# Performance work log

Measured on AMD Instinct MI355X. Metric: run time of the kernel, lower is better.

Reference implementation:

```python
import jax, jax.numpy as jnp
import numpy as np

CUTOFF = 5.2
BOX = 44.0
N_ATOMS = 8192

# 13 half-shifts used by the cell list (vector_index_displacement) + zero shift
HALF_SHIFTS = np.array([
    [-1, 0, 0], [-1, -1, 0], [0, -1, 0], [1, -1, 0],
    [-1, 1, -1], [0, 1, -1], [1, 1, -1], [-1, 0, -1],
    [0, 0, -1], [1, 0, -1], [-1, -1, -1], [0, -1, -1], [1, -1, -1]], dtype=np.int64)
ALL_SHIFTS = np.concatenate([np.zeros((1, 3), dtype=np.int64), HALF_SHIFTS], axis=0)  # (14,3)


def setup_inputs() -> dict:
    key = jax.random.key(0)
    k1, k2 = jax.random.split(key)
    species = jax.random.randint(k1, (1, N_ATOMS), 0, 4, dtype=jnp.int64)
    coordinates = jax.random.uniform(k2, (1, N_ATOMS, 3), dtype=jnp.float32) * BOX
    cell = jnp.eye(3, dtype=jnp.float32) * BOX
    pbc = jnp.ones((3,), dtype=bool)
    return {"species": species, "coordinates": coordinates, "cell": cell, "pbc": pbc}


def reference(species, coordinates, cell, pbc):
    # Single molecule, as asserted by the torch module.
    coords = coordinates[0]  # (N, 3)
    n = coords.shape[0]
    # map_to_central: wrap coordinates into the central cell
    frac = coords @ jnp.linalg.inv(cell)
    frac = frac - jnp.floor(frac)
    coords = frac @ cell
    # orthorhombic cell diagonal (norm of cell columns, as in _setup_variables)
    diag = jnp.linalg.norm(cell, axis=0)  # (3,)

    shifts = jnp.asarray(ALL_SHIFTS)
    pairs_list, shift_list = [], []
    cutoff2 = CUTOFF * CUTOFF
    for k in range(shifts.shape[0]):  # fixed small loop over 14 periodic shifts
        s = shifts[k]
        # delta[i, j] = r_i - r_j + s * cell_diagonal   (N, N, 3)
        delta = coords[:, None, :] - coords[None, :, :] + s.astype(coords.dtype) * diag
        d2 = jnp.sum(delta * delta, axis=-1)  # (N, N)
        mask = d2 <= cutoff2
        if k == 0:
            # within-image pairs: each unordered pair once, no self pairs
            mask = jnp.triu(mask, 1)
        i, j = jnp.nonzero(mask)  # eager: data-dependent pair count
        pairs_list.append(jnp.stack([i, j], axis=0))
        shift_list.append(jnp.broadcast_to(s, (i.shape[0], 3)))
    atom_pairs = jnp.concatenate(pairs_list, axis=1)  # (2, P)
    shift_indices = jnp.concatenate(shift_list, axis=0)  # (P, 3)
    return atom_pairs, shift_indices


if __name__ == "__main__":
    out = reference(**setup_inputs())
    print(out[0].shape, out[1].shape)
```

## Files before the change

### kernel.cpp

```cpp
#include <hip/hip_runtime.h>

#define CLD_NATOMS 8192
#define CLD_NSHIFT 14
#define CLD_NROWS (CLD_NSHIFT * CLD_NATOMS)
#define CLD_NTILE 112
#define CLD_NCELL 512
#define CLD_CAP 128
#define CLD_C2 ((float)(5.2 * 5.2))
#define CLD_R 5.35f

__device__ const int cld_shifts[CLD_NSHIFT][3] = {
    {0, 0, 0},
    {-1, 0, 0}, {-1, -1, 0}, {0, -1, 0}, {1, -1, 0},
    {-1, 1, -1}, {0, 1, -1}, {1, 1, -1}, {-1, 0, -1},
    {0, 0, -1}, {1, 0, -1}, {-1, -1, -1}, {0, -1, -1}, {1, -1, -1}};

__device__ float4 cld_pp[CLD_NATOMS];
__device__ int cld_cid[CLD_NATOMS];
__device__ float4 cld_sorted[CLD_NATOMS];
__device__ unsigned cld_cstart[CLD_NCELL + 1];
__device__ unsigned cld_cfill[CLD_NCELL];
__device__ int cld_jbuf[(size_t)CLD_NROWS * CLD_CAP];
__device__ unsigned cld_cnt[CLD_NROWS];
__device__ unsigned cld_off[CLD_NROWS];
__device__ unsigned cld_tot[CLD_NTILE];
__device__ float4 cld_dg;
__device__ float4 cld_cinv;
__device__ float4 cld_sf[CLD_NSHIFT];

__global__ __launch_bounds__(256) void cld_wrapbin(const float* __restrict__ coords,
                                                   const float* __restrict__ cell) {
  int i = blockIdx.x * blockDim.x + threadIdx.x;
  if (i >= CLD_NATOMS) return;
  float dgx = (float)sqrt((double)cell[0] * cell[0] + (double)cell[3] * cell[3] +
                          (double)cell[6] * cell[6]);
  float dgy = (float)sqrt((double)cell[1] * cell[1] + (double)cell[4] * cell[4] +
                          (double)cell[7] * cell[7]);
  float dgz = (float)sqrt((double)cell[2] * cell[2] + (double)cell[5] * cell[5] +
                          (double)cell[8] * cell[8]);
  float cix = 8.0f / dgx, ciy = 8.0f / dgy, ciz = 8.0f / dgz;
  if (i == 0) {
    cld_dg = make_float4(dgx, dgy, dgz, 0.f);
    cld_cinv = make_float4(cix, ciy, ciz, 0.f);
    for (int k = 0; k < CLD_NSHIFT; ++k)
      cld_sf[k] = make_float4(__fmul_rn((float)cld_shifts[k][0], dgx),
                              __fmul_rn((float)cld_shifts[k][1], dgy),
                              __fmul_rn((float)cld_shifts[k][2], dgz), 0.f);
  }

  double a00 = cell[0], a01 = cell[1], a02 = cell[2];
  double a10 = cell[3], a11 = cell[4], a12 = cell[5];
  double a20 = cell[6], a21 = cell[7], a22 = cell[8];
  double det = a00 * (a11 * a22 - a12 * a21) - a01 * (a10 * a22 - a12 * a20) +
               a02 * (a10 * a21 - a11 * a20);
  double id = 1.0 / det;
  float inv[3][3];
  inv[0][0] = (float)((a11 * a22 - a12 * a21) * id);
  inv[0][1] = (float)(-(a01 * a22 - a02 * a21) * id);
  inv[0][2] = (float)((a01 * a12 - a02 * a11) * id);
  inv[1][0] = (float)(-(a10 * a22 - a12 * a20) * id);
  inv[1][1] = (float)((a00 * a22 - a02 * a20) * id);
  inv[1][2] = (float)(-(a00 * a12 - a02 * a10) * id);
  inv[2][0] = (float)((a10 * a21 - a11 * a20) * id);
  inv[2][1] = (float)(-(a00 * a21 - a01 * a20) * id);
  inv[2][2] = (float)((a00 * a11 - a01 * a10) * id);

  float x = coords[3 * i], y = coords[3 * i + 1], z = coords[3 * i + 2];
  float fr[3], w[3];
#pragma unroll
  for (int c = 0; c < 3; ++c) {
    float f = __fadd_rn(__fadd_rn(__fmul_rn(x, inv[0][c]), __fmul_rn(y, inv[1][c])),
                        __fmul_rn(z, inv[2][c]));
    fr[c] = __fsub_rn(f, floorf(f));
  }
#pragma unroll
  for (int c = 0; c < 3; ++c) {
    w[c] = __fadd_rn(
        __fadd_rn(__fmul_rn(fr[0], cell[0 * 3 + c]), __fmul_rn(fr[1], cell[1 * 3 + c])),
        __fmul_rn(fr[2], cell[2 * 3 + c]));
  }
  cld_pp[i] = make_float4(w[0], w[1], w[2], 0.0f);
  int cx = min(7, (int)(w[0] * cix));
  int cy = min(7, (int)(w[1] * ciy));
  int cz = min(7, (int)(w[2] * ciz));
  cld_cid[i] = (cz * 8 + cy) * 8 + cx;
}

__global__ __launch_bounds__(1024) void cld_cscan() {
  __shared__ unsigned h[CLD_NCELL];
  int t = threadIdx.x;
  if (t < CLD_NCELL) h[t] = 0u;
  __syncthreads();
#pragma unroll
  for (int r = 0; r < 8; ++r) atomicAdd(&h[cld_cid[t + r * 1024]], 1u);
  __syncthreads();
  unsigned v = (t < CLD_NCELL) ? h[t] : 0u;
  unsigned acc = v;
  for (int off = 1; off < CLD_NCELL; off <<= 1) {
    unsigned a = (t >= off && t < CLD_NCELL) ? h[t - off] : 0u;
    __syncthreads();
    if (t < CLD_NCELL) {
      acc += a;
      h[t] = acc;
    }
    __syncthreads();
  }
  if (t < CLD_NCELL) {
    cld_cstart[t] = acc - v;
    cld_cfill[t] = acc - v;
  }
  if (t == CLD_NCELL - 1) cld_cstart[CLD_NCELL] = acc;
}

__global__ __launch_bounds__(256) void cld_scatter() {
  int i = blockIdx.x * blockDim.x + threadIdx.x;
  if (i >= CLD_NATOMS) return;
  unsigned pos = atomicAdd(&cld_cfill[cld_cid[i]], 1u);
  float4 p = cld_pp[i];
  p.w = __int_as_float(i);
  cld_sorted[pos] = p;
}

__device__ __forceinline__ bool cld_alive(float xi, float yi, float zi, int sx, int sy,
                                          int sz, float dgx, float dgy, float dgz) {
  bool a = true;
  if (sx < 0) a = a && (xi >= dgx - 5.3f); else if (sx > 0) a = a && (xi <= 5.3f);
  if (sy < 0) a = a && (yi >= dgy - 5.3f); else if (sy > 0) a = a && (yi <= 5.3f);
  if (sz < 0) a = a && (zi >= dgz - 5.3f); else if (sz > 0) a = a && (zi <= 5.3f);
  return a;
}

__device__ __forceinline__ void cld_crange(float t, float ci, int& lo, int& hi) {
  lo = max(0, (int)(fmaxf(t - CLD_R, 0.f) * ci));
  hi = min(7, (int)(fmaxf(t + CLD_R, 0.f) * ci));
}

__device__ __forceinline__ unsigned cld_iscan(unsigned v, int lane) {
  for (int off = 1; off < 64; off <<= 1) {
    unsigned t = __shfl_up(v, off);
    if (lane >= off) v += t;
  }
  return v;
}

__global__ __launch_bounds__(512) void cld_count() {
  __shared__ uint4 smask[8][64];
  int wslot = threadIdx.x >> 6;
  int wv = blockIdx.x * 8 + wslot;
  int lane = threadIdx.x & 63;
  unsigned* lm = (unsigned*)smask[wslot];
  int k = wv >> 13, i = wv & (CLD_NATOMS - 1);

  float4 dg = cld_dg;
  float4 sc = cld_sf[k];
  int sx = cld_shifts[k][0], sy = cld_shifts[k][1], sz = cld_shifts[k][2];
  float4 pi = cld_pp[i];
  if (k != 0 && !cld_alive(pi.x, pi.y, pi.z, sx, sy, sz, dg.x, dg.y, dg.z)) {
    if (lane == 0) cld_cnt[wv] = 0u;
    return;
  }
  smask[wslot][lane] = make_uint4(0u, 0u, 0u, 0u);

  float4 cinv = cld_cinv;
  int xlo, xhi, ylo, yhi, zlo, zhi;
  cld_crange(__fadd_rn(pi.x, sc.x), cinv.x, xlo, xhi);
  cld_crange(__fadd_rn(pi.y, sc.y), cinv.y, ylo, yhi);
  cld_crange(__fadd_rn(pi.z, sc.z), cinv.z, zlo, zhi);

  for (int cz = zlo; cz <= zhi; ++cz) {
    for (int cy = ylo; cy <= yhi; ++cy) {
      int idb = (cz * 8 + cy) * 8;
      unsigned b = cld_cstart[idb + xlo], e = cld_cstart[idb + xhi + 1];
      for (unsigned t = b + lane; t < e; t += 64) {
        float4 pj = cld_sorted[t];
        int j = __float_as_int(pj.w);
        float dx = __fadd_rn(__fsub_rn(pi.x, pj.x), sc.x);
        float dy = __fadd_rn(__fsub_rn(pi.y, pj.y), sc.y);
        float dz = __fadd_rn(__fsub_rn(pi.z, pj.z), sc.z);
        float d2 = __fadd_rn(__fadd_rn(__fmul_rn(dx, dx), __fmul_rn(dy, dy)),
                             __fmul_rn(dz, dz));
        bool ok = (d2 <= CLD_C2) && (k != 0 || i < j);
        if (ok) atomicOr(&lm[(unsigned)j >> 5], 1u << (j & 31));
      }
    }
  }
  __threadfence_block();

  const unsigned long long* mrow = (const unsigned long long*)lm;
  unsigned long long m0 = mrow[lane];
  unsigned long long m1 = mrow[64 + lane];
  unsigned c0 = (unsigned)__popcll(m0), c1 = (unsigned)__popcll(m1);
  unsigned s0 = cld_iscan(c0, lane);
  unsigned T0 = __shfl(s0, 63);
  unsigned e0 = s0 - c0;
  unsigned s1 = cld_iscan(c1, lane);
  unsigned T1 = __shfl(s1, 63);
  unsigned e1 = T0 + s1 - c1;

  size_t jb = (size_t)wv * CLD_CAP;
  unsigned p = e0;
  unsigned long long m = m0;
  while (m) {
    int b = __ffsll((long long)m) - 1;
    m &= m - 1;
    if (p < CLD_CAP) cld_jbuf[jb + p] = (lane << 6) + b;
    ++p;
  }
  p = e1;
  m = m1;
  while (m) {
    int b = __ffsll((long long)m) - 1;
    m &= m - 1;
    if (p < CLD_CAP) cld_jbuf[jb + p] = ((64 + lane) << 6) + b;
    ++p;
  }
  if (lane == 0) cld_cnt[wv] = min(T0 + T1, (unsigned)CLD_CAP);
}

__global__ __launch_bounds__(1024) void cld_s1() {
  __shared__ unsigned sd[1024];
  int t = threadIdx.x;
  int gid = blockIdx.x * 1024 + t;
  unsigned v = cld_cnt[gid];
  sd[t] = v;
  __syncthreads();
  unsigned acc = v;
  for (int off = 1; off < 1024; off <<= 1) {
    unsigned a = (t >= off) ? sd[t - off] : 0u;
    __syncthreads();
    acc += a;
    sd[t] = acc;
    __syncthreads();
  }
  cld_off[gid] = acc - v;
  if (t == 1023) cld_tot[blockIdx.x] = acc;
}

__global__ __launch_bounds__(512) void cld_emit(int* __restrict__ out, int P) {
  int wv = blockIdx.x * 8 + (threadIdx.x >> 6);
  int lane = threadIdx.x & 63;
  unsigned c = cld_cnt[wv];
  if (c == 0) return;
  int tile = wv >> 10;
  unsigned v = 0;
  if (lane < tile) v = cld_tot[lane];
  if (64 + lane < tile) v += cld_tot[64 + lane];
#pragma unroll
  for (int off = 32; off; off >>= 1) v += __shfl_down(v, off);
  unsigned tbase = __shfl(v, 0);

  unsigned off0 = cld_off[wv] + tbase;
  int k = wv >> 13, i = wv & (CLD_NATOMS - 1);
  int sx = cld_shifts[k][0], sy = cld_shifts[k][1], sz = cld_shifts[k][2];
  size_t jb = (size_t)wv * CLD_CAP;
  for (unsigned q = lane; q < c; q += 64) {
    unsigned p = off0 + q;
    if (p < (unsigned)P) {
      out[p] = i;
      out[P + p] = cld_jbuf[jb + q];
      unsigned sp = 2u * (unsigned)P + 3u * p;
      out[sp] = sx;
      out[sp + 1] = sy;
      out[sp + 2] = sz;
    }
  }
}

extern "C" void kernel_launch(void* const* d_in, const int* in_sizes, int n_in,
                              void* d_out, int out_size, void* d_ws, size_t ws_size,
                              hipStream_t stream) {
  const float* coords = (const float*)d_in[1];
  const float* cell = (const float*)d_in[2];
  int P = out_size / 5;

  cld_wrapbin<<<CLD_NATOMS / 256, 256, 0, stream>>>(coords, cell);
  cld_cscan<<<1, 1024, 0, stream>>>();
  cld_scatter<<<CLD_NATOMS / 256, 256, 0, stream>>>();
  cld_count<<<CLD_NROWS / 8, 512, 0, stream>>>();
  cld_s1<<<CLD_NTILE, 1024, 0, stream>>>();
  cld_emit<<<CLD_NROWS / 8, 512, 0, stream>>>((int*)d_out, P);
}
```

Measured before the change: 53.24 us.

## Compact alive (shift, atom) rows into a work list and use persistent waves

The scatter kernel now evaluates the periodic-boundary liveness test for every shift and appends the surviving rows to a global list with an atomic counter. The count and emit kernels run a fixed grid of persistent waves that stride over this compacted list, so they no longer launch one wave per row across all 14 shifts. Counts are zeroed up front in the wrap kernel so dead rows still scan correctly. The intent is to cut launch and early-exit overhead for the many dead rows. The cost is an extra global atomic plus list writes, and row order in the list is nondeterministic, though output offsets still come from the row-indexed scan.

```diff
diff --git a/kernel.cpp b/kernel.cpp
--- a/kernel.cpp
+++ b/kernel.cpp
@@ -1,37 +1,49 @@
 #include <hip/hip_runtime.h>
 
-#define CLD_NATOMS 8192
-#define CLD_NSHIFT 14
-#define CLD_NROWS (CLD_NSHIFT * CLD_NATOMS)
-#define CLD_NTILE 112
-#define CLD_NCELL 512
-#define CLD_CAP 128
-#define CLD_C2 ((float)(5.2 * 5.2))
-#define CLD_R 5.35f
-
-__device__ const int cld_shifts[CLD_NSHIFT][3] = {
+#define CLF_NATOMS 8192
+#define CLF_NSHIFT 14
+#define CLF_NROWS (CLF_NSHIFT * CLF_NATOMS)
+#define CLF_NTILE 112
+#define CLF_NCELL 512
+#define CLF_CAP 128
+#define CLF_PWAVES 8192
+#define CLF_C2 ((float)(5.2 * 5.2))
+#define CLF_R 5.35f
+
+__device__ const int clf_shifts[CLF_NSHIFT][3] = {
     {0, 0, 0},
     {-1, 0, 0}, {-1, -1, 0}, {0, -1, 0}, {1, -1, 0},
     {-1, 1, -1}, {0, 1, -1}, {1, 1, -1}, {-1, 0, -1},
     {0, 0, -1}, {1, 0, -1}, {-1, -1, -1}, {0, -1, -1}, {1, -1, -1}};
 
-__device__ float4 cld_pp[CLD_NATOMS];
-__device__ int cld_cid[CLD_NATOMS];
-__device__ float4 cld_sorted[CLD_NATOMS];
-__device__ unsigned cld_cstart[CLD_NCELL + 1];
-__device__ unsigned cld_cfill[CLD_NCELL];
-__device__ int cld_jbuf[(size_t)CLD_NROWS * CLD_CAP];
-__device__ unsigned cld_cnt[CLD_NROWS];
-__device__ unsigned cld_off[CLD_NROWS];
-__device__ unsigned cld_tot[CLD_NTILE];
-__device__ float4 cld_dg;
-__device__ float4 cld_cinv;
-__device__ float4 cld_sf[CLD_NSHIFT];
-
-__global__ __launch_bounds__(256) void cld_wrapbin(const float* __restrict__ coords,
+__device__ float4 clf_pp[CLF_NATOMS];
+__device__ int clf_cid[CLF_NATOMS];
+__device__ float4 clf_sorted[CLF_NATOMS];
+__device__ unsigned clf_cstart[CLF_NCELL + 1];
+__device__ unsigned clf_cfill[CLF_NCELL];
+__device__ unsigned clf_nalive;
+__device__ unsigned clf_alist[CLF_NROWS];
+__device__ int clf_jbuf[(size_t)CLF_NROWS * CLF_CAP];
+__device__ unsigned clf_cnt[CLF_NROWS];
+__device__ unsigned clf_off[CLF_NROWS];
+__device__ unsigned clf_tot[CLF_NTILE];
+__device__ float4 clf_dg;
+__device__ float4 clf_cinv;
+__device__ float4 clf_sf[CLF_NSHIFT];
+
+__device__ __forceinline__ bool clf_alive(float xi, float yi, float zi, int sx, int sy,
+                                          int sz, float dgx, float dgy, float dgz) {
+  bool a = true;
+  if (sx < 0) a = a && (xi >= dgx - 5.3f); else if (sx > 0) a = a && (xi <= 5.3f);
+  if (sy < 0) a = a && (yi >= dgy - 5.3f); else if (sy > 0) a = a && (yi <= 5.3f);
+  if (sz < 0) a = a && (zi >= dgz - 5.3f); else if (sz > 0) a = a && (zi <= 5.3f);
+  return a;
+}
+
+__global__ __launch_bounds__(256) void clf_wrapbin(const float* __restrict__ coords,
                                                    const float* __restrict__ cell) {
   int i = blockIdx.x * blockDim.x + threadIdx.x;
-  if (i >= CLD_NATOMS) return;
+  if (i >= CLF_NATOMS) return;
   float dgx = (float)sqrt((double)cell[0] * cell[0] + (double)cell[3] * cell[3] +
                           (double)cell[6] * cell[6]);
   float dgy = (float)sqrt((double)cell[1] * cell[1] + (double)cell[4] * cell[4] +
@@ -40,13 +52,16 @@
                           (double)cell[8] * cell[8]);
   float cix = 8.0f / dgx, ciy = 8.0f / dgy, ciz = 8.0f / dgz;
   if (i == 0) {
-    cld_dg = make_float4(dgx, dgy, dgz, 0.f);
-    cld_cinv = make_float4(cix, ciy, ciz, 0.f);
-    for (int k = 0; k < CLD_NSHIFT; ++k)
-      cld_sf[k] = make_float4(__fmul_rn((float)cld_shifts[k][0], dgx),
-                              __fmul_rn((float)cld_shifts[k][1], dgy),
-                              __fmul_rn((float)cld_shifts[k][2], dgz), 0.f);
-  }
+    clf_dg = make_float4(dgx, dgy, dgz, 0.f);
+    clf_cinv = make_float4(cix, ciy, ciz, 0.f);
+    clf_nalive = 0u;
+    for (int k = 0; k < CLF_NSHIFT; ++k)
+      clf_sf[k] = make_float4(__fmul_rn((float)clf_shifts[k][0], dgx),
+                              __fmul_rn((float)clf_shifts[k][1], dgy),
+                              __fmul_rn((float)clf_shifts[k][2], dgz), 0.f);
+  }
+#pragma unroll
+  for (int k = 0; k < CLF_NSHIFT; ++k) clf_cnt[(k << 13) + i] = 0u;
 
   double a00 = cell[0], a01 = cell[1], a02 = cell[2];
   double a10 = cell[3], a11 = cell[4], a12 = cell[5];
@@ -79,63 +94,68 @@
         __fadd_rn(__fmul_rn(fr[0], cell[0 * 3 + c]), __fmul_rn(fr[1], cell[1 * 3 + c])),
         __fmul_rn(fr[2], cell[2 * 3 + c]));
   }
-  cld_pp[i] = make_float4(w[0], w[1], w[2], 0.0f);
+  clf_pp[i] = make_float4(w[0], w[1], w[2], 0.0f);
   int cx = min(7, (int)(w[0] * cix));
   int cy = min(7, (int)(w[1] * ciy));
   int cz = min(7, (int)(w[2] * ciz));
-  cld_cid[i] = (cz * 8 + cy) * 8 + cx;
-}
-
-__global__ __launch_bounds__(1024) void cld_cscan() {
-  __shared__ unsigned h[CLD_NCELL];
+  clf_cid[i] = (cz * 8 + cy) * 8 + cx;
+}
+
+__global__ __launch_bounds__(1024) void clf_cscan() {
+  __shared__ unsigned h[CLF_NCELL];
   int t = threadIdx.x;
-  if (t < CLD_NCELL) h[t] = 0u;
+  if (t < CLF_NCELL) h[t] = 0u;
   __syncthreads();
 #pragma unroll
-  for (int r = 0; r < 8; ++r) atomicAdd(&h[cld_cid[t + r * 1024]], 1u);
+  for (int r = 0; r < 8; ++r) atomicAdd(&h[clf_cid[t + r * 1024]], 1u);
   __syncthreads();
-  unsigned v = (t < CLD_NCELL) ? h[t] : 0u;
+  unsigned v = (t < CLF_NCELL) ? h[t] : 0u;
   unsigned acc = v;
-  for (int off = 1; off < CLD_NCELL; off <<= 1) {
-    unsigned a = (t >= off && t < CLD_NCELL) ? h[t - off] : 0u;
+  for (int off = 1; off < CLF_NCELL; off <<= 1) {
+    unsigned a = (t >= off && t < CLF_NCELL) ? h[t - off] : 0u;
     __syncthreads();
-    if (t < CLD_NCELL) {
+    if (t < CLF_NCELL) {
       acc += a;
       h[t] = acc;
     }
     __syncthreads();
   }
-  if (t < CLD_NCELL) {
-    cld_cstart[t] = acc - v;
-    cld_cfill[t] = acc - v;
-  }
-  if (t == CLD_NCELL - 1) cld_cstart[CLD_NCELL] = acc;
-}
-
-__global__ __launch_bounds__(256) void cld_scatter() {
+  if (t < CLF_NCELL) {
+    clf_cstart[t] = acc - v;
+    clf_cfill[t] = acc - v;
+  }
+  if (t == CLF_NCELL - 1) clf_cstart[CLF_NCELL] = acc;
+}
+
+__global__ __launch_bounds__(256) void clf_scatter() {
   int i = blockIdx.x * blockDim.x + threadIdx.x;
-  if (i >= CLD_NATOMS) return;
-  unsigned pos = atomicAdd(&cld_cfill[cld_cid[i]], 1u);
-  float4 p = cld_pp[i];
-  p.w = __int_as_float(i);
-  cld_sorted[pos] = p;
-}
-
-__device__ __forceinline__ bool cld_alive(float xi, float yi, float zi, int sx, int sy,
-                                          int sz, float dgx, float dgy, float dgz) {
-  bool a = true;
-  if (sx < 0) a = a && (xi >= dgx - 5.3f); else if (sx > 0) a = a && (xi <= 5.3f);
-  if (sy < 0) a = a && (yi >= dgy - 5.3f); else if (sy > 0) a = a && (yi <= 5.3f);
-  if (sz < 0) a = a && (zi >= dgz - 5.3f); else if (sz > 0) a = a && (zi <= 5.3f);
-  return a;
-}
-
-__device__ __forceinline__ void cld_crange(float t, float ci, int& lo, int& hi) {
-  lo = max(0, (int)(fmaxf(t - CLD_R, 0.f) * ci));
-  hi = min(7, (int)(fmaxf(t + CLD_R, 0.f) * ci));
-}
-
-__device__ __forceinline__ unsigned cld_iscan(unsigned v, int lane) {
+  if (i >= CLF_NATOMS) return;
+  float4 p = clf_pp[i];
+  unsigned pos = atomicAdd(&clf_cfill[clf_cid[i]], 1u);
+  float4 ps = p;
+  ps.w = __int_as_float(i);
+  clf_sorted[pos] = ps;
+
+  float4 dg = clf_dg;
+  unsigned rows[CLF_NSHIFT];
+  int m = 0;
+  rows[m++] = (unsigned)i;
+#pragma unroll
+  for (int k = 1; k < CLF_NSHIFT; ++k) {
+    if (clf_alive(p.x, p.y, p.z, clf_shifts[k][0], clf_shifts[k][1], clf_shifts[k][2],
+                  dg.x, dg.y, dg.z))
+      rows[m++] = (unsigned)((k << 13) + i);
+  }
+  unsigned base = atomicAdd(&clf_nalive, (unsigned)m);
+  for (int q = 0; q < m; ++q) clf_alist[base + q] = rows[q];
+}
+
+__device__ __forceinline__ void clf_crange(float t, float ci, int& lo, int& hi) {
+  lo = max(0, (int)(fmaxf(t - CLF_R, 0.f) * ci));
+  hi = min(7, (int)(fmaxf(t + CLF_R, 0.f) * ci));
+}
+
+__device__ __forceinline__ unsigned clf_iscan(unsigned v, int lane) {
   for (int off = 1; off < 64; off <<= 1) {
     unsigned t = __shfl_up(v, off);
     if (lane >= off) v += t;
@@ -143,85 +163,85 @@
   return v;
 }
 
-__global__ __launch_bounds__(512) void cld_count() {
+__global__ __launch_bounds__(512) void clf_count() {
   __shared__ uint4 smask[8][64];
   int wslot = threadIdx.x >> 6;
-  int wv = blockIdx.x * 8 + wslot;
   int lane = threadIdx.x & 63;
   unsigned* lm = (unsigned*)smask[wslot];
-  int k = wv >> 13, i = wv & (CLD_NATOMS - 1);
-
-  float4 dg = cld_dg;
-  float4 sc = cld_sf[k];
-  int sx = cld_shifts[k][0], sy = cld_shifts[k][1], sz = cld_shifts[k][2];
-  float4 pi = cld_pp[i];
-  if (k != 0 && !cld_alive(pi.x, pi.y, pi.z, sx, sy, sz, dg.x, dg.y, dg.z)) {
-    if (lane == 0) cld_cnt[wv] = 0u;
-    return;
-  }
-  smask[wslot][lane] = make_uint4(0u, 0u, 0u, 0u);
-
-  float4 cinv = cld_cinv;
-  int xlo, xhi, ylo, yhi, zlo, zhi;
-  cld_crange(__fadd_rn(pi.x, sc.x), cinv.x, xlo, xhi);
-  cld_crange(__fadd_rn(pi.y, sc.y), cinv.y, ylo, yhi);
-  cld_crange(__fadd_rn(pi.z, sc.z), cinv.z, zlo, zhi);
-
-  for (int cz = zlo; cz <= zhi; ++cz) {
-    for (int cy = ylo; cy <= yhi; ++cy) {
-      int idb = (cz * 8 + cy) * 8;
-      unsigned b = cld_cstart[idb + xlo], e = cld_cstart[idb + xhi + 1];
-      for (unsigned t = b + lane; t < e; t += 64) {
-        float4 pj = cld_sorted[t];
-        int j = __float_as_int(pj.w);
-        float dx = __fadd_rn(__fsub_rn(pi.x, pj.x), sc.x);
-        float dy = __fadd_rn(__fsub_rn(pi.y, pj.y), sc.y);
-        float dz = __fadd_rn(__fsub_rn(pi.z, pj.z), sc.z);
-        float d2 = __fadd_rn(__fadd_rn(__fmul_rn(dx, dx), __fmul_rn(dy, dy)),
-                             __fmul_rn(dz, dz));
-        bool ok = (d2 <= CLD_C2) && (k != 0 || i < j);
-        if (ok) atomicOr(&lm[(unsigned)j >> 5], 1u << (j & 31));
+  unsigned na = clf_nalive;
+
+  float4 cinv = clf_cinv;
+
+  for (unsigned w = blockIdx.x * 8 + wslot; w < na; w += CLF_PWAVES) {
+    unsigned row = clf_alist[w];
+    int k = row >> 13, i = row & (CLF_NATOMS - 1);
+    float4 sc = clf_sf[k];
+    float4 pi = clf_pp[i];
+    smask[wslot][lane] = make_uint4(0u, 0u, 0u, 0u);
+
+    int xlo, xhi, ylo, yhi, zlo, zhi;
+    clf_crange(__fadd_rn(pi.x, sc.x), cinv.x, xlo, xhi);
+    clf_crange(__fadd_rn(pi.y, sc.y), cinv.y, ylo, yhi);
+    clf_crange(__fadd_rn(pi.z, sc.z), cinv.z, zlo, zhi);
+
+    for (int cz = zlo; cz <= zhi; ++cz) {
+      for (int cy = ylo; cy <= yhi; ++cy) {
+        int idb = (cz * 8 + cy) * 8;
+        unsigned b = clf_cstart[idb + xlo], e = clf_cstart[idb + xhi + 1];
+        for (unsigned t = b + lane; t < e; t += 64) {
+          float4 pj = clf_sorted[t];
+          int j = __float_as_int(pj.w);
+          float dx = __fadd_rn(__fsub_rn(pi.x, pj.x), sc.x);
+          float dy = __fadd_rn(__fsub_rn(pi.y, pj.y), sc.y);
+          float dz = __fadd_rn(__fsub_rn(pi.z, pj.z), sc.z);
+          float d2 = __fadd_rn(__fadd_rn(__fmul_rn(dx, dx), __fmul_rn(dy, dy)),
+                               __fmul_rn(dz, dz));
+          bool ok = (d2 <= CLF_C2) && (k != 0 || i < j);
+          if (ok) atomicOr(&lm[(unsigned)j >> 5], 1u << (j & 31));
+        }
       }
     }
-  }
-  __threadfence_block();
-
-  const unsigned long long* mrow = (const unsigned long long*)lm;
-  unsigned long long m0 = mrow[lane];
-  unsigned long long m1 = mrow[64 + lane];
-  unsigned c0 = (unsigned)__popcll(m0), c1 = (unsigned)__popcll(m1);
-  unsigned s0 = cld_iscan(c0, lane);
-  unsigned T0 = __shfl(s0, 63);
-  unsigned e0 = s0 - c0;
-  unsigned s1 = cld_iscan(c1, lane);
-  unsigned T1 = __shfl(s1, 63);
-  unsigned e1 = T0 + s1 - c1;
-
-  size_t jb = (size_t)wv * CLD_CAP;
-  unsigned p = e0;
-  unsigned long long m = m0;
-  while (m) {
-    int b = __ffsll((long long)m) - 1;
-    m &= m - 1;
-    if (p < CLD_CAP) cld_jbuf[jb + p] = (lane << 6) + b;
-    ++p;
-  }
-  p = e1;
-  m = m1;
-  while (m) {
-    int b = __ffsll((long long)m) - 1;
-    m &= m - 1;
-    if (p < CLD_CAP) cld_jbuf[jb + p] = ((64 + lane) << 6) + b;
-    ++p;
-  }
-  if (lane == 0) cld_cnt[wv] = min(T0 + T1, (unsigned)CLD_CAP);
-}
-
-__global__ __launch_bounds__(1024) void cld_s1() {
+    __threadfence_block();
+
+    const unsigned long long* mrow = (const unsigned long long*)lm;
+    unsigned long long m0 = mrow[lane];
+    unsigned long long m1 = mrow[64 + lane];
+    if (__ballot((m0 | m1) != 0ull) == 0ull) continue;
+
+    unsigned c0 = (unsigned)__popcll(m0), c1 = (unsigned)__popcll(m1);
+    unsigned s0 = clf_iscan(c0, lane);
+    unsigned T0 = __shfl(s0, 63);
+    unsigned e0 = s0 - c0;
+    unsigned s1 = clf_iscan(c1, lane);
+    unsigned T1 = __shfl(s1, 63);
+    unsigned e1 = T0 + s1 - c1;
+
+    size_t jb = (size_t)row * CLF_CAP;
+    unsigned p = e0;
+    unsigned long long m = m0;
+    while (m) {
+      int b = __ffsll((long long)m) - 1;
+      m &= m - 1;
+      if (p < CLF_CAP) clf_jbuf[jb + p] = (lane << 6) + b;
+      ++p;
+    }
+    p = e1;
+    m = m1;
+    while (m) {
+      int b = __ffsll((long long)m) - 1;
+      m &= m - 1;
+      if (p < CLF_CAP) clf_jbuf[jb + p] = ((64 + lane) << 6) + b;
+      ++p;
+    }
+    if (lane == 0) clf_cnt[row] = min(T0 + T1, (unsigned)CLF_CAP);
+  }
+}
+
+__global__ __launch_bounds__(1024) void clf_s1() {
   __shared__ unsigned sd[1024];
   int t = threadIdx.x;
   int gid = blockIdx.x * 1024 + t;
-  unsigned v = cld_cnt[gid];
+  unsigned v = clf_cnt[gid];
   sd[t] = v;
   __syncthreads();
   unsigned acc = v;
@@ -232,36 +252,41 @@
     sd[t] = acc;
     __syncthreads();
   }
-  cld_off[gid] = acc - v;
-  if (t == 1023) cld_tot[blockIdx.x] = acc;
-}
-
-__global__ __launch_bounds__(512) void cld_emit(int* __restrict__ out, int P) {
-  int wv = blockIdx.x * 8 + (threadIdx.x >> 6);
+  clf_off[gid] = acc - v;
+  if (t == 1023) clf_tot[blockIdx.x] = acc;
+}
+
+__global__ __launch_bounds__(512) void clf_emit(int* __restrict__ out, int P) {
+  int wslot = threadIdx.x >> 6;
   int lane = threadIdx.x & 63;
-  unsigned c = cld_cnt[wv];
-  if (c == 0) return;
-  int tile = wv >> 10;
-  unsigned v = 0;
-  if (lane < tile) v = cld_tot[lane];
-  if (64 + lane < tile) v += cld_tot[64 + lane];
-#pragma unroll
-  for (int off = 32; off; off >>= 1) v += __shfl_down(v, off);
-  unsigned tbase = __shfl(v, 0);
-
-  unsigned off0 = cld_off[wv] + tbase;
-  int k = wv >> 13, i = wv & (CLD_NATOMS - 1);
-  int sx = cld_shifts[k][0], sy = cld_shifts[k][1], sz = cld_shifts[k][2];
-  size_t jb = (size_t)wv * CLD_CAP;
-  for (unsigned q = lane; q < c; q += 64) {
-    unsigned p = off0 + q;
-    if (p < (unsigned)P) {
-      out[p] = i;
-      out[P + p] = cld_jbuf[jb + q];
-      unsigned sp = 2u * (unsigned)P + 3u * p;
-      out[sp] = sx;
-      out[sp + 1] = sy;
-      out[sp + 2] = sz;
+  unsigned na = clf_nalive;
+
+  for (unsigned w = blockIdx.x * 8 + wslot; w < na; w += CLF_PWAVES) {
+    unsigned row = clf_alist[w];
+    unsigned c = clf_cnt[row];
+    if (c == 0) continue;
+    int tile = row >> 10;
+    unsigned v = 0;
+    if (lane < tile) v = clf_tot[lane];
+    if (64 + lane < tile) v += clf_tot[64 + lane];
+#pragma unroll
+    for (int off = 32; off; off >>= 1) v += __shfl_down(v, off);
+    unsigned tbase = __shfl(v, 0);
+
+    unsigned off0 = clf_off[row] + tbase;
+    int k = row >> 13, i = row & (CLF_NATOMS - 1);
+    int sx = clf_shifts[k][0], sy = clf_shifts[k][1], sz = clf_shifts[k][2];
+    size_t jb = (size_t)row * CLF_CAP;
+    for (unsigned q = lane; q < c; q += 64) {
+      unsigned p = off0 + q;
+      if (p < (unsigned)P) {
+        out[p] = i;
+        out[P + p] = clf_jbuf[jb + q];
+        unsigned sp = 2u * (unsigned)P + 3u * p;
+        out[sp] = sx;
+        out[sp + 1] = sy;
+        out[sp + 2] = sz;
+      }
     }
   }
 }
@@ -273,10 +298,10 @@
   const float* cell = (const float*)d_in[2];
   int P = out_size / 5;
 
-  cld_wrapbin<<<CLD_NATOMS / 256, 256, 0, stream>>>(coords, cell);
-  cld_cscan<<<1, 1024, 0, stream>>>();
-  cld_scatter<<<CLD_NATOMS / 256, 256, 0, stream>>>();
-  cld_count<<<CLD_NROWS / 8, 512, 0, stream>>>();
-  cld_s1<<<CLD_NTILE, 1024, 0, stream>>>();
-  cld_emit<<<CLD_NROWS / 8, 512, 0, stream>>>((int*)d_out, P);
-}
+  clf_wrapbin<<<CLF_NATOMS / 256, 256, 0, stream>>>(coords, cell);
+  clf_cscan<<<1, 1024, 0, stream>>>();
+  clf_scatter<<<CLF_NATOMS / 256, 256, 0, stream>>>();
+  clf_count<<<CLF_PWAVES / 8, 512, 0, stream>>>();
+  clf_s1<<<CLF_NTILE, 1024, 0, stream>>>();
+  clf_emit<<<CLF_PWAVES / 8, 512, 0, stream>>>((int*)d_out, P);
+}
```

Measured after the change: 45.08 us. 15.3% less time.

## Fuse six-kernel cell-list pipeline into one cooperative persistent kernel with alive-row compaction

Applied to the files above, without the earlier changes.

Replaces the six separate kernel launches with a single cooperative kernel of 256 blocks that separates the wrap/bin, cell scan, scatter, pair counting, prefix scan and emit phases with grid-wide syncs. It also builds a compacted list of alive (atom, shift) rows so that the count and emit phases loop only over rows whose periodic image can reach the box, and skips jbuf writes for rows with no neighbours. This removes launch gaps and the wasted waves on dead rows. In exchange it adds grid.sync overhead, the cell histogram and scan now run on a single block while the rest of the grid waits, and the persistent grid may leave the GPU underoccupied.

```diff
diff --git a/kernel.cpp b/kernel.cpp
--- a/kernel.cpp
+++ b/kernel.cpp
@@ -1,128 +1,45 @@
 #include <hip/hip_runtime.h>
-
-#define CLD_NATOMS 8192
-#define CLD_NSHIFT 14
-#define CLD_NROWS (CLD_NSHIFT * CLD_NATOMS)
-#define CLD_NTILE 112
-#define CLD_NCELL 512
-#define CLD_CAP 128
-#define CLD_C2 ((float)(5.2 * 5.2))
-#define CLD_R 5.35f
-
-__device__ const int cld_shifts[CLD_NSHIFT][3] = {
+#include <hip/hip_cooperative_groups.h>
+
+namespace cg = cooperative_groups;
+
+#define CLG_NATOMS 8192
+#define CLG_NSHIFT 14
+#define CLG_NROWS (CLG_NSHIFT * CLG_NATOMS)
+#define CLG_NTILE 112
+#define CLG_NCELL 512
+#define CLG_CAP 128
+#define CLG_NBLK 256
+#define CLG_NTHR 512
+#define CLG_GSIZE (CLG_NBLK * CLG_NTHR)
+#define CLG_NWAVES (CLG_GSIZE / 64)
+#define CLG_C2 ((float)(5.2 * 5.2))
+#define CLG_R 5.35f
+
+__device__ const int clg_shifts[CLG_NSHIFT][3] = {
     {0, 0, 0},
     {-1, 0, 0}, {-1, -1, 0}, {0, -1, 0}, {1, -1, 0},
     {-1, 1, -1}, {0, 1, -1}, {1, 1, -1}, {-1, 0, -1},
     {0, 0, -1}, {1, 0, -1}, {-1, -1, -1}, {0, -1, -1}, {1, -1, -1}};
 
-__device__ float4 cld_pp[CLD_NATOMS];
-__device__ int cld_cid[CLD_NATOMS];
-__device__ float4 cld_sorted[CLD_NATOMS];
-__device__ unsigned cld_cstart[CLD_NCELL + 1];
-__device__ unsigned cld_cfill[CLD_NCELL];
-__device__ int cld_jbuf[(size_t)CLD_NROWS * CLD_CAP];
-__device__ unsigned cld_cnt[CLD_NROWS];
-__device__ unsigned cld_off[CLD_NROWS];
-__device__ unsigned cld_tot[CLD_NTILE];
-__device__ float4 cld_dg;
-__device__ float4 cld_cinv;
-__device__ float4 cld_sf[CLD_NSHIFT];
-
-__global__ __launch_bounds__(256) void cld_wrapbin(const float* __restrict__ coords,
-                                                   const float* __restrict__ cell) {
-  int i = blockIdx.x * blockDim.x + threadIdx.x;
-  if (i >= CLD_NATOMS) return;
-  float dgx = (float)sqrt((double)cell[0] * cell[0] + (double)cell[3] * cell[3] +
-                          (double)cell[6] * cell[6]);
-  float dgy = (float)sqrt((double)cell[1] * cell[1] + (double)cell[4] * cell[4] +
-                          (double)cell[7] * cell[7]);
-  float dgz = (float)sqrt((double)cell[2] * cell[2] + (double)cell[5] * cell[5] +
-                          (double)cell[8] * cell[8]);
-  float cix = 8.0f / dgx, ciy = 8.0f / dgy, ciz = 8.0f / dgz;
-  if (i == 0) {
-    cld_dg = make_float4(dgx, dgy, dgz, 0.f);
-    cld_cinv = make_float4(cix, ciy, ciz, 0.f);
-    for (int k = 0; k < CLD_NSHIFT; ++k)
-      cld_sf[k] = make_float4(__fmul_rn((float)cld_shifts[k][0], dgx),
-                              __fmul_rn((float)cld_shifts[k][1], dgy),
-                              __fmul_rn((float)cld_shifts[k][2], dgz), 0.f);
-  }
-
-  double a00 = cell[0], a01 = cell[1], a02 = cell[2];
-  double a10 = cell[3], a11 = cell[4], a12 = cell[5];
-  double a20 = cell[6], a21 = cell[7], a22 = cell[8];
-  double det = a00 * (a11 * a22 - a12 * a21) - a01 * (a10 * a22 - a12 * a20) +
-               a02 * (a10 * a21 - a11 * a20);
-  double id = 1.0 / det;
-  float inv[3][3];
-  inv[0][0] = (float)((a11 * a22 - a12 * a21) * id);
-  inv[0][1] = (float)(-(a01 * a22 - a02 * a21) * id);
-  inv[0][2] = (float)((a01 * a12 - a02 * a11) * id);
-  inv[1][0] = (float)(-(a10 * a22 - a12 * a20) * id);
-  inv[1][1] = (float)((a00 * a22 - a02 * a20) * id);
-  inv[1][2] = (float)(-(a00 * a12 - a02 * a10) * id);
-  inv[2][0] = (float)((a10 * a21 - a11 * a20) * id);
-  inv[2][1] = (float)(-(a00 * a21 - a01 * a20) * id);
-  inv[2][2] = (float)((a00 * a11 - a01 * a10) * id);
-
-  float x = coords[3 * i], y = coords[3 * i + 1], z = coords[3 * i + 2];
-  float fr[3], w[3];
-#pragma unroll
-  for (int c = 0; c < 3; ++c) {
-    float f = __fadd_rn(__fadd_rn(__fmul_rn(x, inv[0][c]), __fmul_rn(y, inv[1][c])),
-                        __fmul_rn(z, inv[2][c]));
-    fr[c] = __fsub_rn(f, floorf(f));
-  }
-#pragma unroll
-  for (int c = 0; c < 3; ++c) {
-    w[c] = __fadd_rn(
-        __fadd_rn(__fmul_rn(fr[0], cell[0 * 3 + c]), __fmul_rn(fr[1], cell[1 * 3 + c])),
-        __fmul_rn(fr[2], cell[2 * 3 + c]));
-  }
-  cld_pp[i] = make_float4(w[0], w[1], w[2], 0.0f);
-  int cx = min(7, (int)(w[0] * cix));
-  int cy = min(7, (int)(w[1] * ciy));
-  int cz = min(7, (int)(w[2] * ciz));
-  cld_cid[i] = (cz * 8 + cy) * 8 + cx;
-}
-
-__global__ __launch_bounds__(1024) void cld_cscan() {
-  __shared__ unsigned h[CLD_NCELL];
-  int t = threadIdx.x;
-  if (t < CLD_NCELL) h[t] = 0u;
-  __syncthreads();
-#pragma unroll
-  for (int r = 0; r < 8; ++r) atomicAdd(&h[cld_cid[t + r * 1024]], 1u);
-  __syncthreads();
-  unsigned v = (t < CLD_NCELL) ? h[t] : 0u;
-  unsigned acc = v;
-  for (int off = 1; off < CLD_NCELL; off <<= 1) {
-    unsigned a = (t >= off && t < CLD_NCELL) ? h[t - off] : 0u;
-    __syncthreads();
-    if (t < CLD_NCELL) {
-      acc += a;
-      h[t] = acc;
-    }
-    __syncthreads();
-  }
-  if (t < CLD_NCELL) {
-    cld_cstart[t] = acc - v;
-    cld_cfill[t] = acc - v;
-  }
-  if (t == CLD_NCELL - 1) cld_cstart[CLD_NCELL] = acc;
-}
-
-__global__ __launch_bounds__(256) void cld_scatter() {
-  int i = blockIdx.x * blockDim.x + threadIdx.x;
-  if (i >= CLD_NATOMS) return;
-  unsigned pos = atomicAdd(&cld_cfill[cld_cid[i]], 1u);
-  float4 p = cld_pp[i];
-  p.w = __int_as_float(i);
-  cld_sorted[pos] = p;
-}
-
-__device__ __forceinline__ bool cld_alive(float xi, float yi, float zi, int sx, int sy,
-                                          int sz, float dgx, float dgy, float dgz) {
+__device__ float4 clg_pp[CLG_NATOMS];
+__device__ int clg_cid[CLG_NATOMS];
+__device__ float4 clg_sorted[CLG_NATOMS];
+__device__ unsigned clg_cstart[CLG_NCELL + 1];
+__device__ unsigned clg_cfill[CLG_NCELL];
+__device__ unsigned clg_nalive;
+__device__ unsigned clg_alist[CLG_NROWS];
+__device__ int clg_jbuf[(size_t)CLG_NROWS * CLG_CAP];
+__device__ unsigned clg_cnt[CLG_NROWS];
+__device__ unsigned clg_off[CLG_NROWS];
+__device__ unsigned clg_tot[CLG_NTILE];
+__device__ float4 clg_dg;
+__device__ float4 clg_cinv;
+__device__ float4 clg_sf[CLG_NSHIFT];
+
+__device__ __forceinline__ bool clg_alive_f(float xi, float yi, float zi, int sx,
+                                            int sy, int sz, float dgx, float dgy,
+                                            float dgz) {
   bool a = true;
   if (sx < 0) a = a && (xi >= dgx - 5.3f); else if (sx > 0) a = a && (xi <= 5.3f);
   if (sy < 0) a = a && (yi >= dgy - 5.3f); else if (sy > 0) a = a && (yi <= 5.3f);
@@ -130,12 +47,12 @@
   return a;
 }
 
-__device__ __forceinline__ void cld_crange(float t, float ci, int& lo, int& hi) {
-  lo = max(0, (int)(fmaxf(t - CLD_R, 0.f) * ci));
-  hi = min(7, (int)(fmaxf(t + CLD_R, 0.f) * ci));
-}
-
-__device__ __forceinline__ unsigned cld_iscan(unsigned v, int lane) {
+__device__ __forceinline__ void clg_crange(float t, float ci, int& lo, int& hi) {
+  lo = max(0, (int)(fmaxf(t - CLG_R, 0.f) * ci));
+  hi = min(7, (int)(fmaxf(t + CLG_R, 0.f) * ci));
+}
+
+__device__ __forceinline__ unsigned clg_iscan(unsigned v, int lane) {
   for (int off = 1; off < 64; off <<= 1) {
     unsigned t = __shfl_up(v, off);
     if (lane >= off) v += t;
@@ -143,125 +60,241 @@
   return v;
 }
 
-__global__ __launch_bounds__(512) void cld_count() {
-  __shared__ uint4 smask[8][64];
-  int wslot = threadIdx.x >> 6;
-  int wv = blockIdx.x * 8 + wslot;
-  int lane = threadIdx.x & 63;
-  unsigned* lm = (unsigned*)smask[wslot];
-  int k = wv >> 13, i = wv & (CLD_NATOMS - 1);
-
-  float4 dg = cld_dg;
-  float4 sc = cld_sf[k];
-  int sx = cld_shifts[k][0], sy = cld_shifts[k][1], sz = cld_shifts[k][2];
-  float4 pi = cld_pp[i];
-  if (k != 0 && !cld_alive(pi.x, pi.y, pi.z, sx, sy, sz, dg.x, dg.y, dg.z)) {
-    if (lane == 0) cld_cnt[wv] = 0u;
-    return;
-  }
-  smask[wslot][lane] = make_uint4(0u, 0u, 0u, 0u);
-
-  float4 cinv = cld_cinv;
-  int xlo, xhi, ylo, yhi, zlo, zhi;
-  cld_crange(__fadd_rn(pi.x, sc.x), cinv.x, xlo, xhi);
-  cld_crange(__fadd_rn(pi.y, sc.y), cinv.y, ylo, yhi);
-  cld_crange(__fadd_rn(pi.z, sc.z), cinv.z, zlo, zhi);
-
-  for (int cz = zlo; cz <= zhi; ++cz) {
-    for (int cy = ylo; cy <= yhi; ++cy) {
-      int idb = (cz * 8 + cy) * 8;
-      unsigned b = cld_cstart[idb + xlo], e = cld_cstart[idb + xhi + 1];
-      for (unsigned t = b + lane; t < e; t += 64) {
-        float4 pj = cld_sorted[t];
-        int j = __float_as_int(pj.w);
-        float dx = __fadd_rn(__fsub_rn(pi.x, pj.x), sc.x);
-        float dy = __fadd_rn(__fsub_rn(pi.y, pj.y), sc.y);
-        float dz = __fadd_rn(__fsub_rn(pi.z, pj.z), sc.z);
-        float d2 = __fadd_rn(__fadd_rn(__fmul_rn(dx, dx), __fmul_rn(dy, dy)),
-                             __fmul_rn(dz, dz));
-        bool ok = (d2 <= CLD_C2) && (k != 0 || i < j);
-        if (ok) atomicOr(&lm[(unsigned)j >> 5], 1u << (j & 31));
+__global__ __launch_bounds__(CLG_NTHR) void clg_fused(const float* __restrict__ coords,
+                                                      const float* __restrict__ cell,
+                                                      int* __restrict__ out, int P) {
+  cg::grid_group grid = cg::this_grid();
+  __shared__ union {
+    unsigned h[CLG_NCELL];
+    uint4 smask[8][64];
+    unsigned sd[CLG_NTHR];
+  } shm;
+
+  int tid = threadIdx.x;
+  int gid = blockIdx.x * CLG_NTHR + tid;
+  int lane = tid & 63;
+  int wslot = tid >> 6;
+
+  if (gid < CLG_NROWS) clg_cnt[gid] = 0u;
+  if (gid < CLG_NATOMS) {
+    float dgx = (float)sqrt((double)cell[0] * cell[0] + (double)cell[3] * cell[3] +
+                            (double)cell[6] * cell[6]);
+    float dgy = (float)sqrt((double)cell[1] * cell[1] + (double)cell[4] * cell[4] +
+                            (double)cell[7] * cell[7]);
+    float dgz = (float)sqrt((double)cell[2] * cell[2] + (double)cell[5] * cell[5] +
+                            (double)cell[8] * cell[8]);
+    float cix = 8.0f / dgx, ciy = 8.0f / dgy, ciz = 8.0f / dgz;
+    if (gid == 0) {
+      clg_dg = make_float4(dgx, dgy, dgz, 0.f);
+      clg_cinv = make_float4(cix, ciy, ciz, 0.f);
+      clg_nalive = 0u;
+      for (int k = 0; k < CLG_NSHIFT; ++k)
+        clg_sf[k] = make_float4(__fmul_rn((float)clg_shifts[k][0], dgx),
+                                __fmul_rn((float)clg_shifts[k][1], dgy),
+                                __fmul_rn((float)clg_shifts[k][2], dgz), 0.f);
+    }
+    double a00 = cell[0], a01 = cell[1], a02 = cell[2];
+    double a10 = cell[3], a11 = cell[4], a12 = cell[5];
+    double a20 = cell[6], a21 = cell[7], a22 = cell[8];
+    double det = a00 * (a11 * a22 - a12 * a21) - a01 * (a10 * a22 - a12 * a20) +
+                 a02 * (a10 * a21 - a11 * a20);
+    double id = 1.0 / det;
+    float inv[3][3];
+    inv[0][0] = (float)((a11 * a22 - a12 * a21) * id);
+    inv[0][1] = (float)(-(a01 * a22 - a02 * a21) * id);
+    inv[0][2] = (float)((a01 * a12 - a02 * a11) * id);
+    inv[1][0] = (float)(-(a10 * a22 - a12 * a20) * id);
+    inv[1][1] = (float)((a00 * a22 - a02 * a20) * id);
+    inv[1][2] = (float)(-(a00 * a12 - a02 * a10) * id);
+    inv[2][0] = (float)((a10 * a21 - a11 * a20) * id);
+    inv[2][1] = (float)(-(a00 * a21 - a01 * a20) * id);
+    inv[2][2] = (float)((a00 * a11 - a01 * a10) * id);
+
+    float x = coords[3 * gid], y = coords[3 * gid + 1], z = coords[3 * gid + 2];
+    float fr[3], w[3];
+#pragma unroll
+    for (int c = 0; c < 3; ++c) {
+      float f = __fadd_rn(__fadd_rn(__fmul_rn(x, inv[0][c]), __fmul_rn(y, inv[1][c])),
+                          __fmul_rn(z, inv[2][c]));
+      fr[c] = __fsub_rn(f, floorf(f));
+    }
+#pragma unroll
+    for (int c = 0; c < 3; ++c) {
+      w[c] = __fadd_rn(__fadd_rn(__fmul_rn(fr[0], cell[0 * 3 + c]),
+                                 __fmul_rn(fr[1], cell[1 * 3 + c])),
+                       __fmul_rn(fr[2], cell[2 * 3 + c]));
+    }
+    clg_pp[gid] = make_float4(w[0], w[1], w[2], 0.0f);
+    int cx = min(7, (int)(w[0] * cix));
+    int cy = min(7, (int)(w[1] * ciy));
+    int cz = min(7, (int)(w[2] * ciz));
+    clg_cid[gid] = (cz * 8 + cy) * 8 + cx;
+  }
+  grid.sync();
+
+  if (blockIdx.x == 0) {
+    shm.h[tid] = 0u;
+    __syncthreads();
+    for (int r = tid; r < CLG_NATOMS; r += CLG_NTHR) atomicAdd(&shm.h[clg_cid[r]], 1u);
+    __syncthreads();
+    unsigned v = shm.h[tid];
+    unsigned acc = v;
+    for (int off = 1; off < CLG_NCELL; off <<= 1) {
+      unsigned a = (tid >= off) ? shm.h[tid - off] : 0u;
+      __syncthreads();
+      acc += a;
+      shm.h[tid] = acc;
+      __syncthreads();
+    }
+    clg_cstart[tid] = acc - v;
+    clg_cfill[tid] = acc - v;
+    if (tid == CLG_NCELL - 1) clg_cstart[CLG_NCELL] = acc;
+  }
+  grid.sync();
+
+  if (gid < CLG_NATOMS) {
+    float4 p = clg_pp[gid];
+    unsigned pos = atomicAdd(&clg_cfill[clg_cid[gid]], 1u);
+    float4 ps = p;
+    ps.w = __int_as_float(gid);
+    clg_sorted[pos] = ps;
+
+    float4 dg = clg_dg;
+    unsigned rows[CLG_NSHIFT];
+    int m = 0;
+    rows[m++] = (unsigned)gid;
+#pragma unroll
+    for (int k = 1; k < CLG_NSHIFT; ++k) {
+      if (clg_alive_f(p.x, p.y, p.z, clg_shifts[k][0], clg_shifts[k][1],
+                      clg_shifts[k][2], dg.x, dg.y, dg.z))
+        rows[m++] = (unsigned)((k << 13) + gid);
+    }
+    unsigned base = atomicAdd(&clg_nalive, (unsigned)m);
+    for (int q = 0; q < m; ++q) clg_alist[base + q] = rows[q];
+  }
+  grid.sync();
+
+  {
+    unsigned na = clg_nalive;
+    float4 cinv = clg_cinv;
+    unsigned* lm = (unsigned*)shm.smask[wslot];
+
+    for (unsigned w = blockIdx.x * 8 + wslot; w < na; w += CLG_NWAVES) {
+      unsigned row = clg_alist[w];
+      int k = row >> 13, i = row & (CLG_NATOMS - 1);
+      float4 sc = clg_sf[k];
+      float4 pi = clg_pp[i];
+      shm.smask[wslot][lane] = make_uint4(0u, 0u, 0u, 0u);
+
+      int xlo, xhi, ylo, yhi, zlo, zhi;
+      clg_crange(__fadd_rn(pi.x, sc.x), cinv.x, xlo, xhi);
+      clg_crange(__fadd_rn(pi.y, sc.y), cinv.y, ylo, yhi);
+      clg_crange(__fadd_rn(pi.z, sc.z), cinv.z, zlo, zhi);
+
+      for (int cz = zlo; cz <= zhi; ++cz) {
+        for (int cy = ylo; cy <= yhi; ++cy) {
+          int idb = (cz * 8 + cy) * 8;
+          unsigned b = clg_cstart[idb + xlo], e = clg_cstart[idb + xhi + 1];
+          for (unsigned t = b + lane; t < e; t += 64) {
+            float4 pj = clg_sorted[t];
+            int j = __float_as_int(pj.w);
+            float dx = __fadd_rn(__fsub_rn(pi.x, pj.x), sc.x);
+            float dy = __fadd_rn(__fsub_rn(pi.y, pj.y), sc.y);
+            float dz = __fadd_rn(__fsub_rn(pi.z, pj.z), sc.z);
+            float d2 = __fadd_rn(__fadd_rn(__fmul_rn(dx, dx), __fmul_rn(dy, dy)),
+                                 __fmul_rn(dz, dz));
+            bool ok = (d2 <= CLG_C2) && (k != 0 || i < j);
+            if (ok) atomicOr(&lm[(unsigned)j >> 5], 1u << (j & 31));
+          }
+        }
       }
-    }
-  }
-  __threadfence_block();
-
-  const unsigned long long* mrow = (const unsigned long long*)lm;
-  unsigned long long m0 = mrow[lane];
-  unsigned long long m1 = mrow[64 + lane];
-  unsigned c0 = (unsigned)__popcll(m0), c1 = (unsigned)__popcll(m1);
-  unsigned s0 = cld_iscan(c0, lane);
-  unsigned T0 = __shfl(s0, 63);
-  unsigned e0 = s0 - c0;
-  unsigned s1 = cld_iscan(c1, lane);
-  unsigned T1 = __shfl(s1, 63);
-  unsigned e1 = T0 + s1 - c1;
-
-  size_t jb = (size_t)wv * CLD_CAP;
-  unsigned p = e0;
-  unsigned long long m = m0;
-  while (m) {
-    int b = __ffsll((long long)m) - 1;
-    m &= m - 1;
-    if (p < CLD_CAP) cld_jbuf[jb + p] = (lane << 6) + b;
-    ++p;
-  }
-  p = e1;
-  m = m1;
-  while (m) {
-    int b = __ffsll((long long)m) - 1;
-    m &= m - 1;
-    if (p < CLD_CAP) cld_jbuf[jb + p] = ((64 + lane) << 6) + b;
-    ++p;
-  }
-  if (lane == 0) cld_cnt[wv] = min(T0 + T1, (unsigned)CLD_CAP);
-}
-
-__global__ __launch_bounds__(1024) void cld_s1() {
-  __shared__ unsigned sd[1024];
-  int t = threadIdx.x;
-  int gid = blockIdx.x * 1024 + t;
-  unsigned v = cld_cnt[gid];
-  sd[t] = v;
-  __syncthreads();
-  unsigned acc = v;
-  for (int off = 1; off < 1024; off <<= 1) {
-    unsigned a = (t >= off) ? sd[t - off] : 0u;
+      __threadfence_block();
+
+      const unsigned long long* mrow = (const unsigned long long*)lm;
+      unsigned long long m0 = mrow[lane];
+      unsigned long long m1 = mrow[64 + lane];
+      if (__ballot((m0 | m1) != 0ull) == 0ull) continue;
+
+      unsigned c0 = (unsigned)__popcll(m0), c1 = (unsigned)__popcll(m1);
+      unsigned s0 = clg_iscan(c0, lane);
+      unsigned T0 = __shfl(s0, 63);
+      unsigned e0 = s0 - c0;
+      unsigned s1 = clg_iscan(c1, lane);
+      unsigned T1 = __shfl(s1, 63);
+      unsigned e1 = T0 + s1 - c1;
+
+      size_t jb = (size_t)row * CLG_CAP;
+      unsigned p = e0;
+      unsigned long long m = m0;
+      while (m) {
+        int b = __ffsll((long long)m) - 1;
+        m &= m - 1;
+        if (p < CLG_CAP) clg_jbuf[jb + p] = (lane << 6) + b;
+        ++p;
+      }
+      p = e1;
+      m = m1;
+      while (m) {
+        int b = __ffsll((long long)m) - 1;
+        m &= m - 1;
+        if (p < CLG_CAP) clg_jbuf[jb + p] = ((64 + lane) << 6) + b;
+        ++p;
+      }
+      if (lane == 0) clg_cnt[row] = min(T0 + T1, (unsigned)CLG_CAP);
+    }
+  }
+  grid.sync();
+
+  if (blockIdx.x < CLG_NTILE) {
+    int base = blockIdx.x * 1024;
+    unsigned v0 = clg_cnt[base + 2 * tid], v1 = clg_cnt[base + 2 * tid + 1];
+    unsigned ps = v0 + v1;
+    shm.sd[tid] = ps;
     __syncthreads();
-    acc += a;
-    sd[t] = acc;
-    __syncthreads();
-  }
-  cld_off[gid] = acc - v;
-  if (t == 1023) cld_tot[blockIdx.x] = acc;
-}
-
-__global__ __launch_bounds__(512) void cld_emit(int* __restrict__ out, int P) {
-  int wv = blockIdx.x * 8 + (threadIdx.x >> 6);
-  int lane = threadIdx.x & 63;
-  unsigned c = cld_cnt[wv];
-  if (c == 0) return;
-  int tile = wv >> 10;
-  unsigned v = 0;
-  if (lane < tile) v = cld_tot[lane];
-  if (64 + lane < tile) v += cld_tot[64 + lane];
+    unsigned acc = ps;
+    for (int off = 1; off < CLG_NTHR; off <<= 1) {
+      unsigned a = (tid >= off) ? shm.sd[tid - off] : 0u;
+      __syncthreads();
+      acc += a;
+      shm.sd[tid] = acc;
+      __syncthreads();
+    }
+    unsigned pb = acc - ps;
+    clg_off[base + 2 * tid] = pb;
+    clg_off[base + 2 * tid + 1] = pb + v0;
+    if (tid == CLG_NTHR - 1) clg_tot[blockIdx.x] = acc;
+  }
+  grid.sync();
+
+  {
+    unsigned na = clg_nalive;
+    for (unsigned w = blockIdx.x * 8 + wslot; w < na; w += CLG_NWAVES) {
+      unsigned row = clg_alist[w];
+      unsigned c = clg_cnt[row];
+      if (c == 0) continue;
+      int tile = row >> 10;
+      unsigned v = 0;
+      if (lane < tile) v = clg_tot[lane];
+      if (64 + lane < tile) v += clg_tot[64 + lane];
 #pragma unroll
-  for (int off = 32; off; off >>= 1) v += __shfl_down(v, off);
-  unsigned tbase = __shfl(v, 0);
-
-  unsigned off0 = cld_off[wv] + tbase;
-  int k = wv >> 13, i = wv & (CLD_NATOMS - 1);
-  int sx = cld_shifts[k][0], sy = cld_shifts[k][1], sz = cld_shifts[k][2];
-  size_t jb = (size_t)wv * CLD_CAP;
-  for (unsigned q = lane; q < c; q += 64) {
-    unsigned p = off0 + q;
-    if (p < (unsigned)P) {
-      out[p] = i;
-      out[P + p] = cld_jbuf[jb + q];
-      unsigned sp = 2u * (unsigned)P + 3u * p;
-      out[sp] = sx;
-      out[sp + 1] = sy;
-      out[sp + 2] = sz;
+      for (int off = 32; off; off >>= 1) v += __shfl_down(v, off);
+      unsigned tbase = __shfl(v, 0);
+
+      unsigned off0 = clg_off[row] + tbase;
+      int k = row >> 13, i = row & (CLG_NATOMS - 1);
+      int sx = clg_shifts[k][0], sy = clg_shifts[k][1], sz = clg_shifts[k][2];
+      size_t jb = (size_t)row * CLG_CAP;
+      for (unsigned q = lane; q < c; q += 64) {
+        unsigned p = off0 + q;
+        if (p < (unsigned)P) {
+          out[p] = i;
+          out[P + p] = clg_jbuf[jb + q];
+          unsigned sp = 2u * (unsigned)P + 3u * p;
+          out[sp] = sx;
+          out[sp + 1] = sy;
+          out[sp + 2] = sz;
+        }
+      }
     }
   }
 }
@@ -271,12 +304,10 @@
                               hipStream_t stream) {
   const float* coords = (const float*)d_in[1];
   const float* cell = (const float*)d_in[2];
+  int* outp = (int*)d_out;
   int P = out_size / 5;
 
-  cld_wrapbin<<<CLD_NATOMS / 256, 256, 0, stream>>>(coords, cell);
-  cld_cscan<<<1, 1024, 0, stream>>>();
-  cld_scatter<<<CLD_NATOMS / 256, 256, 0, stream>>>();
-  cld_count<<<CLD_NROWS / 8, 512, 0, stream>>>();
-  cld_s1<<<CLD_NTILE, 1024, 0, stream>>>();
-  cld_emit<<<CLD_NROWS / 8, 512, 0, stream>>>((int*)d_out, P);
-}
+  void* args[] = {(void*)&coords, (void*)&cell, (void*)&outp, (void*)&P};
+  hipLaunchCooperativeKernel((const void*)clg_fused, dim3(CLG_NBLK), dim3(CLG_NTHR),
+                             args, 0, stream);
+}
```

Measured after the change: 193.7 us. 3.64x slower.
